# Kernel optimization log

Measured on AMD Instinct MI355X. Metric: run time of the kernel, lower is better.

The kernel has to match this reference:

```python
import jax, jax.numpy as jnp
import numpy as np

B, N, IN_DIM, HID = 64, 1024, 128, 32


def _xavier(key, shape):
    # xavier_uniform_ on torch Linear weight [out, in]; we store [in, out]
    fan_in, fan_out = shape[0], shape[1]
    limit = float(np.sqrt(6.0 / (fan_in + fan_out)))
    return jax.random.uniform(key, shape, jnp.float32, -limit, limit)


def setup_inputs() -> dict:
    key = jax.random.key(0)
    ks = jax.random.split(key, 8)
    x = jax.random.normal(ks[0], (B, N, IN_DIM), jnp.float32)
    adj = jax.random.uniform(ks[1], (B, N, N), jnp.float32)  # dense adjacency
    W1 = _xavier(ks[2], (IN_DIM, HID))
    W2 = _xavier(ks[3], (HID, HID))
    W3 = _xavier(ks[4], (HID, HID))
    W4 = _xavier(ks[5], (HID, HID))
    b1 = jnp.zeros((HID,), jnp.float32)
    b2 = jnp.zeros((HID,), jnp.float32)
    b3 = jnp.zeros((HID,), jnp.float32)
    b4 = jnp.zeros((HID,), jnp.float32)
    a1 = jnp.float32(0.25)  # PReLU default init
    a2 = jnp.float32(0.25)
    a3 = jnp.float32(0.25)
    a4 = jnp.float32(0.25)
    return {"x": x, "adj": adj, "W1": W1, "W2": W2, "W3": W3, "W4": W4,
            "b1": b1, "b2": b2, "b3": b3, "b4": b4,
            "a1": a1, "a2": a2, "a3": a3, "a4": a4}


def _gcn_layer(x, adj, W, b, a):
    h = jnp.einsum('bnf,fo->bno', x, W)      # linear, no bias
    h = jnp.matmul(adj, h) + b               # aggregation + bias
    return jnp.where(h >= 0, h, a * h)       # PReLU


def reference(x, adj, W1, W2, W3, W4, b1, b2, b3, b4, a1, a2, a3, a4):
    h1 = _gcn_layer(x, adj, W1, b1, a1)
    h2 = _gcn_layer(h1, adj, W2, b2, a2)
    h3 = _gcn_layer(h2, adj, W3, b3, a3)
    h4 = _gcn_layer(h3, adj, W4, b4, a4)
    # sum-pool nodes per layer, concat along feature dim -> [B, 4*HID]
    return jnp.concatenate([h1.sum(axis=1), h2.sum(axis=1),
                            h3.sum(axis=1), h4.sum(axis=1)], axis=1)
```

## Files before the change

### kernel.cpp

```cpp
#include <hip/hip_runtime.h>
#include <hip/hip_bf16.h>

#define B_   64
#define N_   1024
#define IND_ 128
#define HID_ 32

typedef __attribute__((ext_vector_type(8))) short short8;
typedef __attribute__((ext_vector_type(4))) float f32x4;
typedef __attribute__((ext_vector_type(4))) unsigned int u32x4;
typedef unsigned short u16;

static __device__ __forceinline__ u16 f2bf(float f) {
    union { float f; unsigned int u; } v; v.f = f;
    unsigned int r = v.u + 0x7FFFu + ((v.u >> 16) & 1u);
    return (u16)(r >> 16);
}

template<int F>
__global__ __launch_bounds__(256) void linear_kernel(
    const float* __restrict__ in,
    const float* __restrict__ W,
    u16* __restrict__ outT)
{
    __shared__ float sW[F][HID_];
    const int tid = threadIdx.x;
    for (int e = tid; e < F * HID_; e += 256) sW[e / HID_][e % HID_] = W[e];
    __syncthreads();

    const int b = blockIdx.x >> 2;
    const int n = ((blockIdx.x & 3) << 8) + tid;
    const f32x4* row4 = (const f32x4*)(in + ((size_t)b * N_ + n) * F);

    float acc[HID_];
#pragma unroll
    for (int o = 0; o < HID_; ++o) acc[o] = 0.f;

#pragma unroll 4
    for (int f4 = 0; f4 < F / 4; ++f4) {
        f32x4 xv = row4[f4];
#pragma unroll
        for (int j = 0; j < 4; ++j) {
#pragma unroll
            for (int o = 0; o < HID_; ++o) acc[o] += xv[j] * sW[f4 * 4 + j][o];
        }
    }
    u16* op = outT + (size_t)b * HID_ * N_ + n;
#pragma unroll
    for (int o = 0; o < HID_; ++o) op[o * N_] = f2bf(acc[o]);
}

union AggSmem {
    u16   sB[HID_][N_ + 8];
    float h_s[128][33];
};

template<int MODE, int FUSE>
__global__ __launch_bounds__(256) void agg_kernel(
    const float* __restrict__ adjf,
    const u16*  __restrict__ adjb_in,
    u16*        __restrict__ adjb_out,
    const u16*  __restrict__ hlinT_in,
    u16*        __restrict__ hlinT_out,
    const float* __restrict__ Wnext,
    float*      __restrict__ h,
    float*      __restrict__ partial,
    const float* __restrict__ bias,
    const float* __restrict__ alpha_p)
{
    __shared__ AggSmem sm;
    __shared__ float pool[4][HID_];
    __shared__ float sW2[HID_][HID_];
    const int tid = threadIdx.x;
    const int b = blockIdx.y;

    if (FUSE) {
        for (int e = tid; e < HID_ * HID_; e += 256) sW2[e >> 5][e & 31] = Wnext[e];
    }
    {
        const u32x4* src = (const u32x4*)(hlinT_in + (size_t)b * HID_ * N_);
        for (int i = tid; i < (HID_ * N_) / 8; i += 256) {
            int c = (i * 8) >> 10;
            int k = (i * 8) & (N_ - 1);
            *(u32x4*)&sm.sB[c][k] = src[i];
        }
    }
    __syncthreads();

    const int wid = tid >> 6, lane = tid & 63;
    const int r16 = lane & 15, g = lane >> 4;
    const int koff = g * 8;
    const int rowbase = blockIdx.x * 128 + wid * 32;
    const int row0 = rowbase + r16;
    const int row1 = row0 + 16;
    const size_t adj_b = (size_t)b * N_ * N_;

    f32x4 acc[2][2] = {};

    for (int k0 = 0; k0 < N_; k0 += 32) {
        short8 a0, a1;
        if (MODE == 0) {
            a0 = *(const short8*)&adjb_in[adj_b + (size_t)row0 * N_ + k0 + koff];
            a1 = *(const short8*)&adjb_in[adj_b + (size_t)row1 * N_ + k0 + koff];
        } else {
            const f32x4* p0 = (const f32x4*)(adjf + adj_b + (size_t)row0 * N_ + k0 + koff);
            const f32x4* p1 = (const f32x4*)(adjf + adj_b + (size_t)row1 * N_ + k0 + koff);
            f32x4 v00 = __builtin_nontemporal_load(p0);
            f32x4 v01 = __builtin_nontemporal_load(p0 + 1);
            f32x4 v10 = __builtin_nontemporal_load(p1);
            f32x4 v11 = __builtin_nontemporal_load(p1 + 1);
#pragma unroll
            for (int i = 0; i < 4; ++i) {
                a0[i]     = (short)f2bf(v00[i]);
                a0[i + 4] = (short)f2bf(v01[i]);
                a1[i]     = (short)f2bf(v10[i]);
                a1[i + 4] = (short)f2bf(v11[i]);
            }
            if (MODE == 1) {
                *(short8*)&adjb_out[adj_b + (size_t)row0 * N_ + k0 + koff] = a0;
                *(short8*)&adjb_out[adj_b + (size_t)row1 * N_ + k0 + koff] = a1;
            }
        }
        short8 b0 = *(const short8*)&sm.sB[r16][k0 + koff];
        short8 b1 = *(const short8*)&sm.sB[16 + r16][k0 + koff];
        acc[0][0] = __builtin_amdgcn_mfma_f32_16x16x32_bf16(a0, b0, acc[0][0], 0, 0, 0);
        acc[0][1] = __builtin_amdgcn_mfma_f32_16x16x32_bf16(a0, b1, acc[0][1], 0, 0, 0);
        acc[1][0] = __builtin_amdgcn_mfma_f32_16x16x32_bf16(a1, b0, acc[1][0], 0, 0, 0);
        acc[1][1] = __builtin_amdgcn_mfma_f32_16x16x32_bf16(a1, b1, acc[1][1], 0, 0, 0);
    }

    const float alpha = *alpha_p;
    float v[2][2][4];
    float ps[2];
#pragma unroll
    for (int ct = 0; ct < 2; ++ct) {
        const float bv = bias[ct * 16 + r16];
        ps[ct] = 0.f;
#pragma unroll
        for (int rt = 0; rt < 2; ++rt) {
#pragma unroll
            for (int r = 0; r < 4; ++r) {
                float x = acc[rt][ct][r] + bv;
                x = (x >= 0.f) ? x : alpha * x;
                v[ct][rt][r] = x;
                ps[ct] += x;
            }
        }
    }
    __syncthreads();

#pragma unroll
    for (int ct = 0; ct < 2; ++ct) {
        const int col = ct * 16 + r16;
        float p = ps[ct];
        p += __shfl_xor(p, 16, 64);
        p += __shfl_xor(p, 32, 64);
        if (lane < 16) pool[wid][col] = p;
        if (FUSE) {
#pragma unroll
            for (int rt = 0; rt < 2; ++rt)
#pragma unroll
                for (int r = 0; r < 4; ++r)
                    sm.h_s[wid * 32 + rt * 16 + g * 4 + r][col] = v[ct][rt][r];
        }
        if (MODE == 2) {
#pragma unroll
            for (int rt = 0; rt < 2; ++rt)
#pragma unroll
                for (int r = 0; r < 4; ++r) {
                    const int row = rowbase + rt * 16 + g * 4 + r;
                    h[((size_t)b * N_ + row) * HID_ + col] = v[ct][rt][r];
                }
        }
    }
    __syncthreads();

    if (tid < HID_) {
        float s = pool[0][tid] + pool[1][tid] + pool[2][tid] + pool[3][tid];
        partial[((size_t)b * 8 + blockIdx.x) * HID_ + tid] = s;
    }

    if (FUSE) {
        const int r_local = tid >> 1;
        const int obase = (tid & 1) * 16;
        float acc2[16];
#pragma unroll
        for (int o = 0; o < 16; ++o) acc2[o] = 0.f;
#pragma unroll 4
        for (int k = 0; k < HID_; ++k) {
            const float hv = sm.h_s[r_local][k];
#pragma unroll
            for (int o = 0; o < 16; ++o) acc2[o] += hv * sW2[k][obase + o];
        }
        const int n = blockIdx.x * 128 + r_local;
        u16* op = hlinT_out + (size_t)b * HID_ * N_ + n;
#pragma unroll
        for (int o = 0; o < 16; ++o) op[(size_t)(obase + o) * N_] = f2bf(acc2[o]);
    }
}

__global__ __launch_bounds__(256) void finalize_kernel(
    const float* __restrict__ partial,
    float* __restrict__ out)
{
    const int i = blockIdx.x * 256 + threadIdx.x;
    if (i >= B_ * 4 * HID_) return;
    const int b = i >> 7;
    const int rem = i & 127;
    const int l = rem >> 5;
    const int o = rem & 31;
    const float* p = partial + (((size_t)l * B_ + b) * 8) * HID_ + o;
    float s = 0.f;
#pragma unroll
    for (int t = 0; t < 8; ++t) s += p[t * HID_];
    out[i] = s;
}

extern "C" void kernel_launch(void* const* d_in, const int* in_sizes, int n_in,
                              void* d_out, int out_size, void* d_ws, size_t ws_size,
                              hipStream_t stream) {
    const float* x   = (const float*)d_in[0];
    const float* adj = (const float*)d_in[1];
    const float* W[4]  = {(const float*)d_in[2], (const float*)d_in[3],
                          (const float*)d_in[4], (const float*)d_in[5]};
    const float* bi[4] = {(const float*)d_in[6], (const float*)d_in[7],
                          (const float*)d_in[8], (const float*)d_in[9]};
    const float* al[4] = {(const float*)d_in[10], (const float*)d_in[11],
                          (const float*)d_in[12], (const float*)d_in[13]};
    float* out = (float*)d_out;

    const size_t adjb_bytes = (size_t)B_ * N_ * N_ * 2;
    const size_t hlin_bytes = (size_t)B_ * HID_ * N_ * 2;
    const size_t h_bytes    = (size_t)B_ * N_ * HID_ * 4;
    const size_t part_bytes = (size_t)4 * B_ * 8 * HID_ * 4;
    const bool full = ws_size >= adjb_bytes + 2 * hlin_bytes + part_bytes;

    const dim3 ga(8, 64);
    const int part_stride = B_ * 8 * HID_;

    if (full) {
        char* p = (char*)d_ws;
        u16* adjb  = (u16*)p;  p += adjb_bytes;
        u16* hlinA = (u16*)p;  p += hlin_bytes;
        u16* hlinB = (u16*)p;  p += hlin_bytes;
        float* partial = (float*)p;

        linear_kernel<IND_><<<256, 256, 0, stream>>>(x, W[0], hlinA);
        agg_kernel<1, 1><<<ga, 256, 0, stream>>>(adj, nullptr, adjb, hlinA, hlinB,
                                                 W[1], nullptr,
                                                 partial + 0, bi[0], al[0]);
        agg_kernel<0, 1><<<ga, 256, 0, stream>>>(nullptr, adjb, nullptr, hlinB, hlinA,
                                                 W[2], nullptr,
                                                 partial + (size_t)1 * part_stride,
                                                 bi[1], al[1]);
        agg_kernel<0, 1><<<ga, 256, 0, stream>>>(nullptr, adjb, nullptr, hlinA, hlinB,
                                                 W[3], nullptr,
                                                 partial + (size_t)2 * part_stride,
                                                 bi[2], al[2]);
        agg_kernel<0, 0><<<ga, 256, 0, stream>>>(nullptr, adjb, nullptr, hlinB, nullptr,
                                                 nullptr, nullptr,
                                                 partial + (size_t)3 * part_stride,
                                                 bi[3], al[3]);
    } else {
        char* p = (char*)d_ws;
        u16*   hlinT   = (u16*)p;  p += hlin_bytes;
        float* h       = (float*)p; p += h_bytes;
        float* partial = (float*)p;

        linear_kernel<IND_><<<256, 256, 0, stream>>>(x, W[0], hlinT);
        agg_kernel<2, 0><<<ga, 256, 0, stream>>>(adj, nullptr, nullptr, hlinT, nullptr,
                                                 nullptr, h, partial + 0, bi[0], al[0]);
        for (int l = 1; l < 4; ++l) {
            linear_kernel<HID_><<<256, 256, 0, stream>>>(h, W[l], hlinT);
            agg_kernel<2, 0><<<ga, 256, 0, stream>>>(adj, nullptr, nullptr, hlinT, nullptr,
                                                     nullptr, h,
                                                     partial + (size_t)l * part_stride,
                                                     bi[l], al[l]);
        }
    }
    finalize_kernel<<<32, 256, 0, stream>>>(
        (const float*)((char*)d_ws + (full ? adjb_bytes + 2 * hlin_bytes
                                           : hlin_bytes + h_bytes)), out);
}
```

Measured before the change: 222.3 us.

## Read aggregation B-operand directly from global instead of staging in LDS

```diff
diff --git a/kernel.cpp b/kernel.cpp
--- a/kernel.cpp
+++ b/kernel.cpp
@@ -8,7 +8,6 @@
 
 typedef __attribute__((ext_vector_type(8))) short short8;
 typedef __attribute__((ext_vector_type(4))) float f32x4;
-typedef __attribute__((ext_vector_type(4))) unsigned int u32x4;
 typedef unsigned short u16;
 
 static __device__ __forceinline__ u16 f2bf(float f) {
@@ -50,13 +49,8 @@
     for (int o = 0; o < HID_; ++o) op[o * N_] = f2bf(acc[o]);
 }
 
-union AggSmem {
-    u16   sB[HID_][N_ + 8];
-    float h_s[128][33];
-};
-
 template<int MODE, int FUSE>
-__global__ __launch_bounds__(256) void agg_kernel(
+__global__ __launch_bounds__(256, 5) void agg_kernel(
     const float* __restrict__ adjf,
     const u16*  __restrict__ adjb_in,
     u16*        __restrict__ adjb_out,
@@ -68,47 +62,54 @@
     const float* __restrict__ bias,
     const float* __restrict__ alpha_p)
 {
-    __shared__ AggSmem sm;
     __shared__ float pool[4][HID_];
-    __shared__ float sW2[HID_][HID_];
+    __shared__ float h_s[FUSE ? 128 : 1][33];
+    __shared__ float sW2[FUSE ? HID_ : 1][HID_];
     const int tid = threadIdx.x;
     const int b = blockIdx.y;
 
     if (FUSE) {
         for (int e = tid; e < HID_ * HID_; e += 256) sW2[e >> 5][e & 31] = Wnext[e];
     }
-    {
-        const u32x4* src = (const u32x4*)(hlinT_in + (size_t)b * HID_ * N_);
-        for (int i = tid; i < (HID_ * N_) / 8; i += 256) {
-            int c = (i * 8) >> 10;
-            int k = (i * 8) & (N_ - 1);
-            *(u32x4*)&sm.sB[c][k] = src[i];
-        }
-    }
-    __syncthreads();
 
     const int wid = tid >> 6, lane = tid & 63;
     const int r16 = lane & 15, g = lane >> 4;
     const int koff = g * 8;
     const int rowbase = blockIdx.x * 128 + wid * 32;
     const int row0 = rowbase + r16;
-    const int row1 = row0 + 16;
     const size_t adj_b = (size_t)b * N_ * N_;
 
+    const u16* pb0 = hlinT_in + (size_t)b * HID_ * N_ + (size_t)r16 * N_ + koff;
+    const u16* pb1 = pb0 + 16 * N_;
+
     f32x4 acc[2][2] = {};
 
-    for (int k0 = 0; k0 < N_; k0 += 32) {
-        short8 a0, a1;
-        if (MODE == 0) {
-            a0 = *(const short8*)&adjb_in[adj_b + (size_t)row0 * N_ + k0 + koff];
-            a1 = *(const short8*)&adjb_in[adj_b + (size_t)row1 * N_ + k0 + koff];
-        } else {
-            const f32x4* p0 = (const f32x4*)(adjf + adj_b + (size_t)row0 * N_ + k0 + koff);
-            const f32x4* p1 = (const f32x4*)(adjf + adj_b + (size_t)row1 * N_ + k0 + koff);
-            f32x4 v00 = __builtin_nontemporal_load(p0);
-            f32x4 v01 = __builtin_nontemporal_load(p0 + 1);
-            f32x4 v10 = __builtin_nontemporal_load(p1);
-            f32x4 v11 = __builtin_nontemporal_load(p1 + 1);
+    if (MODE == 0) {
+        const u16* pa0 = adjb_in + adj_b + (size_t)row0 * N_ + koff;
+        const u16* pa1 = pa0 + 16 * N_;
+#pragma unroll 2
+        for (int k0 = 0; k0 < N_; k0 += 32) {
+            short8 a0 = *(const short8*)(pa0 + k0);
+            short8 a1 = *(const short8*)(pa1 + k0);
+            short8 b0 = *(const short8*)(pb0 + k0);
+            short8 b1 = *(const short8*)(pb1 + k0);
+            acc[0][0] = __builtin_amdgcn_mfma_f32_16x16x32_bf16(a0, b0, acc[0][0], 0, 0, 0);
+            acc[0][1] = __builtin_amdgcn_mfma_f32_16x16x32_bf16(a0, b1, acc[0][1], 0, 0, 0);
+            acc[1][0] = __builtin_amdgcn_mfma_f32_16x16x32_bf16(a1, b0, acc[1][0], 0, 0, 0);
+            acc[1][1] = __builtin_amdgcn_mfma_f32_16x16x32_bf16(a1, b1, acc[1][1], 0, 0, 0);
+        }
+    } else {
+        const float* pf0 = adjf + adj_b + (size_t)row0 * N_ + koff;
+        const float* pf1 = pf0 + 16 * N_;
+        u16* po0 = (MODE == 1) ? adjb_out + adj_b + (size_t)row0 * N_ + koff : nullptr;
+        u16* po1 = (MODE == 1) ? po0 + 16 * N_ : nullptr;
+#pragma unroll 2
+        for (int k0 = 0; k0 < N_; k0 += 32) {
+            f32x4 v00 = __builtin_nontemporal_load((const f32x4*)(pf0 + k0));
+            f32x4 v01 = __builtin_nontemporal_load((const f32x4*)(pf0 + k0) + 1);
+            f32x4 v10 = __builtin_nontemporal_load((const f32x4*)(pf1 + k0));
+            f32x4 v11 = __builtin_nontemporal_load((const f32x4*)(pf1 + k0) + 1);
+            short8 a0, a1;
 #pragma unroll
             for (int i = 0; i < 4; ++i) {
                 a0[i]     = (short)f2bf(v00[i]);
@@ -117,16 +118,16 @@
                 a1[i + 4] = (short)f2bf(v11[i]);
             }
             if (MODE == 1) {
-                *(short8*)&adjb_out[adj_b + (size_t)row0 * N_ + k0 + koff] = a0;
-                *(short8*)&adjb_out[adj_b + (size_t)row1 * N_ + k0 + koff] = a1;
+                *(short8*)(po0 + k0) = a0;
+                *(short8*)(po1 + k0) = a1;
             }
-        }
-        short8 b0 = *(const short8*)&sm.sB[r16][k0 + koff];
-        short8 b1 = *(const short8*)&sm.sB[16 + r16][k0 + koff];
-        acc[0][0] = __builtin_amdgcn_mfma_f32_16x16x32_bf16(a0, b0, acc[0][0], 0, 0, 0);
-        acc[0][1] = __builtin_amdgcn_mfma_f32_16x16x32_bf16(a0, b1, acc[0][1], 0, 0, 0);
-        acc[1][0] = __builtin_amdgcn_mfma_f32_16x16x32_bf16(a1, b0, acc[1][0], 0, 0, 0);
-        acc[1][1] = __builtin_amdgcn_mfma_f32_16x16x32_bf16(a1, b1, acc[1][1], 0, 0, 0);
+            short8 b0 = *(const short8*)(pb0 + k0);
+            short8 b1 = *(const short8*)(pb1 + k0);
+            acc[0][0] = __builtin_amdgcn_mfma_f32_16x16x32_bf16(a0, b0, acc[0][0], 0, 0, 0);
+            acc[0][1] = __builtin_amdgcn_mfma_f32_16x16x32_bf16(a0, b1, acc[0][1], 0, 0, 0);
+            acc[1][0] = __builtin_amdgcn_mfma_f32_16x16x32_bf16(a1, b0, acc[1][0], 0, 0, 0);
+            acc[1][1] = __builtin_amdgcn_mfma_f32_16x16x32_bf16(a1, b1, acc[1][1], 0, 0, 0);
+        }
     }
 
     const float alpha = *alpha_p;
@@ -147,7 +148,6 @@
             }
         }
     }
-    __syncthreads();
 
 #pragma unroll
     for (int ct = 0; ct < 2; ++ct) {
@@ -161,7 +161,7 @@
             for (int rt = 0; rt < 2; ++rt)
 #pragma unroll
                 for (int r = 0; r < 4; ++r)
-                    sm.h_s[wid * 32 + rt * 16 + g * 4 + r][col] = v[ct][rt][r];
+                    h_s[wid * 32 + rt * 16 + g * 4 + r][col] = v[ct][rt][r];
         }
         if (MODE == 2) {
 #pragma unroll
@@ -188,7 +188,7 @@
         for (int o = 0; o < 16; ++o) acc2[o] = 0.f;
 #pragma unroll 4
         for (int k = 0; k < HID_; ++k) {
-            const float hv = sm.h_s[r_local][k];
+            const float hv = h_s[r_local][k];
 #pragma unroll
             for (int o = 0; o < 16; ++o) acc2[o] += hv * sW2[k][obase + o];
         }
```

After: 249.1 us. 1.12x slower.

## Halve agg block rows and stage hidden features in two K chunks

Applied to the files above, without the earlier changes.

```diff
diff --git a/kernel.cpp b/kernel.cpp
--- a/kernel.cpp
+++ b/kernel.cpp
@@ -8,7 +8,6 @@
 
 typedef __attribute__((ext_vector_type(8))) short short8;
 typedef __attribute__((ext_vector_type(4))) float f32x4;
-typedef __attribute__((ext_vector_type(4))) unsigned int u32x4;
 typedef unsigned short u16;
 
 static __device__ __forceinline__ u16 f2bf(float f) {
@@ -49,11 +48,6 @@
 #pragma unroll
     for (int o = 0; o < HID_; ++o) op[o * N_] = f2bf(acc[o]);
 }
-
-union AggSmem {
-    u16   sB[HID_][N_ + 8];
-    float h_s[128][33];
-};
 
 template<int MODE, int FUSE>
 __global__ __launch_bounds__(256) void agg_kernel(
@@ -68,85 +62,78 @@
     const float* __restrict__ bias,
     const float* __restrict__ alpha_p)
 {
-    __shared__ AggSmem sm;
+    union Smem {
+        u16 sB[HID_][512 + 8];
+        struct { float h_s[64][33]; float sW2[HID_][HID_]; } ep;
+    };
+    __shared__ Smem sm;
     __shared__ float pool[4][HID_];
-    __shared__ float sW2[HID_][HID_];
+
     const int tid = threadIdx.x;
     const int b = blockIdx.y;
-
-    if (FUSE) {
-        for (int e = tid; e < HID_ * HID_; e += 256) sW2[e >> 5][e & 31] = Wnext[e];
-    }
-    {
-        const u32x4* src = (const u32x4*)(hlinT_in + (size_t)b * HID_ * N_);
-        for (int i = tid; i < (HID_ * N_) / 8; i += 256) {
-            int c = (i * 8) >> 10;
-            int k = (i * 8) & (N_ - 1);
-            *(u32x4*)&sm.sB[c][k] = src[i];
-        }
-    }
-    __syncthreads();
-
     const int wid = tid >> 6, lane = tid & 63;
     const int r16 = lane & 15, g = lane >> 4;
     const int koff = g * 8;
-    const int rowbase = blockIdx.x * 128 + wid * 32;
+    const int rowbase = blockIdx.x * 64 + wid * 16;
     const int row0 = rowbase + r16;
-    const int row1 = row0 + 16;
     const size_t adj_b = (size_t)b * N_ * N_;
-
-    f32x4 acc[2][2] = {};
-
-    for (int k0 = 0; k0 < N_; k0 += 32) {
-        short8 a0, a1;
-        if (MODE == 0) {
-            a0 = *(const short8*)&adjb_in[adj_b + (size_t)row0 * N_ + k0 + koff];
-            a1 = *(const short8*)&adjb_in[adj_b + (size_t)row1 * N_ + k0 + koff];
-        } else {
-            const f32x4* p0 = (const f32x4*)(adjf + adj_b + (size_t)row0 * N_ + k0 + koff);
-            const f32x4* p1 = (const f32x4*)(adjf + adj_b + (size_t)row1 * N_ + k0 + koff);
-            f32x4 v00 = __builtin_nontemporal_load(p0);
-            f32x4 v01 = __builtin_nontemporal_load(p0 + 1);
-            f32x4 v10 = __builtin_nontemporal_load(p1);
-            f32x4 v11 = __builtin_nontemporal_load(p1 + 1);
-#pragma unroll
-            for (int i = 0; i < 4; ++i) {
-                a0[i]     = (short)f2bf(v00[i]);
-                a0[i + 4] = (short)f2bf(v01[i]);
-                a1[i]     = (short)f2bf(v10[i]);
-                a1[i + 4] = (short)f2bf(v11[i]);
+    const u16* srcB = hlinT_in + (size_t)b * HID_ * N_;
+
+    const u16*  pa = adjb_in  ? adjb_in  + adj_b + (size_t)row0 * N_ + koff : nullptr;
+    const float* pf = adjf    ? adjf     + adj_b + (size_t)row0 * N_ + koff : nullptr;
+    u16*        po = adjb_out ? adjb_out + adj_b + (size_t)row0 * N_ + koff : nullptr;
+
+    f32x4 acc[2] = {};
+
+    for (int c = 0; c < 2; ++c) {
+        if (c) __syncthreads();
+        for (int i = tid; i < 2048; i += 256) {
+            const int row = i >> 6;
+            const int kv = (i & 63) << 3;
+            *(short8*)&sm.sB[row][kv] =
+                *(const short8*)(srcB + (size_t)row * N_ + (c << 9) + kv);
+        }
+        __syncthreads();
+
+#pragma unroll 4
+        for (int kk = 0; kk < 512; kk += 32) {
+            const int k0 = (c << 9) + kk;
+            short8 a0;
+            if (MODE == 0) {
+                a0 = *(const short8*)(pa + k0);
+            } else {
+                f32x4 v0 = __builtin_nontemporal_load((const f32x4*)(pf + k0));
+                f32x4 v1 = __builtin_nontemporal_load((const f32x4*)(pf + k0) + 1);
+#pragma unroll
+                for (int i = 0; i < 4; ++i) {
+                    a0[i]     = (short)f2bf(v0[i]);
+                    a0[i + 4] = (short)f2bf(v1[i]);
+                }
+                if (MODE == 1) *(short8*)(po + k0) = a0;
             }
-            if (MODE == 1) {
-                *(short8*)&adjb_out[adj_b + (size_t)row0 * N_ + k0 + koff] = a0;
-                *(short8*)&adjb_out[adj_b + (size_t)row1 * N_ + k0 + koff] = a1;
-            }
-        }
-        short8 b0 = *(const short8*)&sm.sB[r16][k0 + koff];
-        short8 b1 = *(const short8*)&sm.sB[16 + r16][k0 + koff];
-        acc[0][0] = __builtin_amdgcn_mfma_f32_16x16x32_bf16(a0, b0, acc[0][0], 0, 0, 0);
-        acc[0][1] = __builtin_amdgcn_mfma_f32_16x16x32_bf16(a0, b1, acc[0][1], 0, 0, 0);
-        acc[1][0] = __builtin_amdgcn_mfma_f32_16x16x32_bf16(a1, b0, acc[1][0], 0, 0, 0);
-        acc[1][1] = __builtin_amdgcn_mfma_f32_16x16x32_bf16(a1, b1, acc[1][1], 0, 0, 0);
+            short8 b0 = *(const short8*)&sm.sB[r16][kk + koff];
+            short8 b1 = *(const short8*)&sm.sB[16 + r16][kk + koff];
+            acc[0] = __builtin_amdgcn_mfma_f32_16x16x32_bf16(a0, b0, acc[0], 0, 0, 0);
+            acc[1] = __builtin_amdgcn_mfma_f32_16x16x32_bf16(a0, b1, acc[1], 0, 0, 0);
+        }
     }
 
     const float alpha = *alpha_p;
-    float v[2][2][4];
+    float v[2][4];
     float ps[2];
 #pragma unroll
     for (int ct = 0; ct < 2; ++ct) {
         const float bv = bias[ct * 16 + r16];
         ps[ct] = 0.f;
 #pragma unroll
-        for (int rt = 0; rt < 2; ++rt) {
-#pragma unroll
-            for (int r = 0; r < 4; ++r) {
-                float x = acc[rt][ct][r] + bv;
-                x = (x >= 0.f) ? x : alpha * x;
-                v[ct][rt][r] = x;
-                ps[ct] += x;
-            }
-        }
-    }
+        for (int r = 0; r < 4; ++r) {
+            float x = acc[ct][r] + bv;
+            x = (x >= 0.f) ? x : alpha * x;
+            v[ct][r] = x;
+            ps[ct] += x;
+        }
+    }
+
     __syncthreads();
 
 #pragma unroll
@@ -158,44 +145,44 @@
         if (lane < 16) pool[wid][col] = p;
         if (FUSE) {
 #pragma unroll
-            for (int rt = 0; rt < 2; ++rt)
-#pragma unroll
-                for (int r = 0; r < 4; ++r)
-                    sm.h_s[wid * 32 + rt * 16 + g * 4 + r][col] = v[ct][rt][r];
+            for (int r = 0; r < 4; ++r)
+                sm.ep.h_s[wid * 16 + g * 4 + r][col] = v[ct][r];
         }
         if (MODE == 2) {
 #pragma unroll
-            for (int rt = 0; rt < 2; ++rt)
-#pragma unroll
-                for (int r = 0; r < 4; ++r) {
-                    const int row = rowbase + rt * 16 + g * 4 + r;
-                    h[((size_t)b * N_ + row) * HID_ + col] = v[ct][rt][r];
-                }
-        }
+            for (int r = 0; r < 4; ++r) {
+                const int row = rowbase + g * 4 + r;
+                h[((size_t)b * N_ + row) * HID_ + col] = v[ct][r];
+            }
+        }
+    }
+    if (FUSE) {
+        for (int e = tid; e < HID_ * HID_; e += 256)
+            ((float*)sm.ep.sW2)[e] = Wnext[e];
     }
     __syncthreads();
 
     if (tid < HID_) {
         float s = pool[0][tid] + pool[1][tid] + pool[2][tid] + pool[3][tid];
-        partial[((size_t)b * 8 + blockIdx.x) * HID_ + tid] = s;
+        partial[((size_t)b * 16 + blockIdx.x) * HID_ + tid] = s;
     }
 
     if (FUSE) {
-        const int r_local = tid >> 1;
-        const int obase = (tid & 1) * 16;
-        float acc2[16];
-#pragma unroll
-        for (int o = 0; o < 16; ++o) acc2[o] = 0.f;
+        const int r_local = tid >> 2;
+        const int obase = (tid & 3) * 8;
+        float acc2[8];
+#pragma unroll
+        for (int o = 0; o < 8; ++o) acc2[o] = 0.f;
 #pragma unroll 4
         for (int k = 0; k < HID_; ++k) {
-            const float hv = sm.h_s[r_local][k];
-#pragma unroll
-            for (int o = 0; o < 16; ++o) acc2[o] += hv * sW2[k][obase + o];
-        }
-        const int n = blockIdx.x * 128 + r_local;
+            const float hv = sm.ep.h_s[r_local][k];
+#pragma unroll
+            for (int o = 0; o < 8; ++o) acc2[o] += hv * sm.ep.sW2[k][obase + o];
+        }
+        const int n = blockIdx.x * 64 + r_local;
         u16* op = hlinT_out + (size_t)b * HID_ * N_ + n;
 #pragma unroll
-        for (int o = 0; o < 16; ++o) op[(size_t)(obase + o) * N_] = f2bf(acc2[o]);
+        for (int o = 0; o < 8; ++o) op[(size_t)(obase + o) * N_] = f2bf(acc2[o]);
     }
 }
 
@@ -209,10 +196,10 @@
     const int rem = i & 127;
     const int l = rem >> 5;
     const int o = rem & 31;
-    const float* p = partial + (((size_t)l * B_ + b) * 8) * HID_ + o;
+    const float* p = partial + (((size_t)l * B_ + b) * 16) * HID_ + o;
     float s = 0.f;
 #pragma unroll
-    for (int t = 0; t < 8; ++t) s += p[t * HID_];
+    for (int t = 0; t < 16; ++t) s += p[t * HID_];
     out[i] = s;
 }
 
@@ -232,11 +219,11 @@
     const size_t adjb_bytes = (size_t)B_ * N_ * N_ * 2;
     const size_t hlin_bytes = (size_t)B_ * HID_ * N_ * 2;
     const size_t h_bytes    = (size_t)B_ * N_ * HID_ * 4;
-    const size_t part_bytes = (size_t)4 * B_ * 8 * HID_ * 4;
+    const size_t part_bytes = (size_t)4 * B_ * 16 * HID_ * 4;
     const bool full = ws_size >= adjb_bytes + 2 * hlin_bytes + part_bytes;
 
-    const dim3 ga(8, 64);
-    const int part_stride = B_ * 8 * HID_;
+    const dim3 ga(16, 64);
+    const int part_stride = B_ * 16 * HID_;
 
     if (full) {
         char* p = (char*)d_ws;
```

Result: faster. 213.3 us (-4.1%).
